# Optimization experiments

Measured on AMD Instinct MI355X. Metric: run time of the kernel, lower is better.

The kernel has to match this reference:

```python
import jax, jax.numpy as jnp
import numpy as np

B, H, L, N = 16, 128, 4096, 64
DT_MIN, DT_MAX = 0.001, 0.1


def _make_dplr_hippo(n):
    # NPLR HiPPO -> DPLR diagonalization (numpy, init-time only)
    p0 = np.sqrt(1 + 2 * np.arange(n))
    A = p0[:, None] * p0[None, :]
    A = -(np.tril(A) - np.diag(np.arange(n)))
    p = np.sqrt(np.arange(n) + 0.5)
    b = np.sqrt(2 * np.arange(n) + 1.0)
    S = A + p[:, None] * p[None, :]
    Lam_re = np.mean(np.diagonal(S)) * np.ones(n)
    Lam_im, V = np.linalg.eigh(S * -1j)
    p = V.conj().T @ p
    b = V.conj().T @ b
    return Lam_re + 1j * Lam_im, p, b


def setup_inputs() -> dict:
    key = jax.random.key(0)
    k1, k2, k3 = jax.random.split(key, 3)
    Lam, p, b = _make_dplr_hippo(N)
    tile = lambda a: jnp.tile(jnp.asarray(a, jnp.float32)[None], (H, 1))
    Lambda_re = tile(Lam.real)
    Lambda_im = tile(Lam.imag)
    P_ri = jnp.tile(jnp.stack([jnp.asarray(p.real, jnp.float32), jnp.asarray(p.imag, jnp.float32)], -1)[None], (H, 1, 1))
    B_ri = jnp.tile(jnp.stack([jnp.asarray(b.real, jnp.float32), jnp.asarray(b.imag, jnp.float32)], -1)[None], (H, 1, 1))
    C = (0.5 ** 0.5) * jax.random.normal(k1, (H, N, 2), jnp.float32)
    log_step = jax.random.uniform(k2, (H,)) * (np.log(DT_MAX) - np.log(DT_MIN)) + np.log(DT_MIN)
    D = jnp.ones((H,), jnp.float32)
    u = jax.random.normal(k3, (B, H, L), jnp.float32)
    return {"u": u, "Lambda_re": Lambda_re, "Lambda_im": Lambda_im, "P_ri": P_ri,
            "B_ri": B_ri, "C": C, "log_step": log_step.astype(jnp.float32), "D": D}


def reference(u, Lambda_re, Lambda_im, P_ri, B_ri, C, log_step, D):
    Lseq = u.shape[-1]
    # setup(): Lambda = clip(Lambda_re, max=-1e-4) + i*Lambda_im ; C complex ; step = exp(log_step)
    Lam = jnp.minimum(Lambda_re, -1e-4) + 1j * Lambda_im            # [H,N]
    P = P_ri[..., 0] + 1j * P_ri[..., 1]                             # [H,N]
    Bm = B_ri[..., 0] + 1j * B_ri[..., 1]                            # [H,N]
    Cc = C[..., 0] + 1j * C[..., 1]                                  # [H,N]
    step = jnp.exp(log_step)                                         # [H]
    # kernel_DPLR at the roots of unity
    Omega = jnp.exp(-2j * jnp.pi * (jnp.arange(Lseq) / Lseq))        # [L]
    g = (2.0 / step)[:, None] * ((1.0 - Omega) / (1.0 + Omega))[None, :]  # [H,L]
    c = 2.0 / (1.0 + Omega)                                          # [L]
    den = 1.0 / (g[:, :, None] - Lam[:, None, :])                    # [H,L,N] resolvent
    # four Cauchy dot products, batched: v stacked on last axis
    Vmat = jnp.stack([Cc.conj() * Bm, Cc.conj() * P, P.conj() * Bm, P.conj() * P], axis=-1)  # [H,N,4]
    Ks = jnp.einsum('hln,hnk->hlk', den, Vmat)                       # [H,L,4]
    k00, k01, k10, k11 = Ks[..., 0], Ks[..., 1], Ks[..., 2], Ks[..., 3]
    atRoots = c[None, :] * (k00 - k01 * (1.0 / (1.0 + k11)) * k10)   # [H,L]
    K = jnp.fft.ifft(atRoots, Lseq, axis=-1).real                    # [H,L] SSM kernel
    # causal FFT convolution: pad both to 2L
    ud = jnp.fft.rfft(jnp.pad(u, ((0, 0), (0, 0), (0, Lseq))), axis=-1)   # [B,H,L+1]
    Kd = jnp.fft.rfft(jnp.pad(K, ((0, 0), (0, Lseq))), axis=-1)           # [H,L+1]
    y = jnp.fft.irfft(ud * Kd[None], axis=-1)[..., :Lseq]            # [B,H,L]
    return y + D[None, :, None] * u
```

## Files before the change

### kernel.cpp

```cpp
#include <hip/hip_runtime.h>
#include <hip/hip_bf16.h>


#define PI_F 3.14159265358979323846f

__device__ __forceinline__ float2 cmulf(float2 a, float2 b) {
  return make_float2(a.x * b.x - a.y * b.y, a.x * b.y + a.y * b.x);
}
__device__ __forceinline__ void cmul_set(float2& v, float wr, float wi) {
  v = make_float2(v.x * wr - v.y * wi, v.x * wi + v.y * wr);
}
__device__ __forceinline__ int ad(int k) { return k + (k >> 4); }
__device__ __forceinline__ int sw16(int j) { return j ^ ((j >> 4) & 15); }

template <int SIGN>
__device__ __forceinline__ void bfly4(float2& a, float2& b, float2& c,
                                      float2& d) {
  float t0x = a.x + c.x, t0y = a.y + c.y;
  float t1x = a.x - c.x, t1y = a.y - c.y;
  float t2x = b.x + d.x, t2y = b.y + d.y;
  float t3x = b.x - d.x, t3y = b.y - d.y;
  a = make_float2(t0x + t2x, t0y + t2y);
  c = make_float2(t0x - t2x, t0y - t2y);
  if (SIGN < 0) {
    b = make_float2(t1x + t3y, t1y - t3x);
    d = make_float2(t1x - t3y, t1y + t3x);
  } else {
    b = make_float2(t1x - t3y, t1y + t3x);
    d = make_float2(t1x + t3y, t1y - t3x);
  }
}

template <int SIGN>
__device__ __forceinline__ void fft16(float2 v[16]) {
  const float sg = (float)SIGN;
  const float C1 = 0.92387953251128674f;
  const float S1 = 0.38268343236508978f;
  const float R2 = 0.70710678118654752f;
  bfly4<SIGN>(v[0], v[4], v[8], v[12]);
  bfly4<SIGN>(v[1], v[5], v[9], v[13]);
  bfly4<SIGN>(v[2], v[6], v[10], v[14]);
  bfly4<SIGN>(v[3], v[7], v[11], v[15]);
  cmul_set(v[5], C1, sg * S1);
  cmul_set(v[6], R2, sg * R2);
  cmul_set(v[7], S1, sg * C1);
  cmul_set(v[9], R2, sg * R2);
  v[10] = make_float2(-sg * v[10].y, sg * v[10].x);
  cmul_set(v[11], -R2, sg * R2);
  cmul_set(v[13], S1, sg * C1);
  cmul_set(v[14], -R2, sg * R2);
  cmul_set(v[15], -C1, -sg * S1);
  float2 w[16];
#pragma unroll
  for (int g = 0; g < 4; ++g) {
    float2 x0 = v[4 * g], x1 = v[4 * g + 1], x2 = v[4 * g + 2],
           x3 = v[4 * g + 3];
    bfly4<SIGN>(x0, x1, x2, x3);
    w[g] = x0; w[g + 4] = x1; w[g + 8] = x2; w[g + 12] = x3;
  }
#pragma unroll
  for (int i = 0; i < 16; ++i) v[i] = w[i];
}

__device__ __forceinline__ void tw_apply(float2 v[16], float ang) {
  float sn, cn;
  __sincosf(ang, &sn, &cn);
  float2 w1 = make_float2(cn, sn), cw = w1;
#pragma unroll
  for (int g = 1; g < 16; ++g) {
    v[g] = cmulf(v[g], cw);
    if (g < 15) cw = cmulf(cw, w1);
  }
}

template <int SIGN>
__device__ void fft4096_regs(float2 v[16], float2* lds, int tid) {
  const int a = tid & 15, g2 = tid >> 4;
  fft16<SIGN>(v);
  tw_apply(v, (float)SIGN * (2.0f * PI_F / 4096.0f) * (float)tid);
  __syncthreads();
#pragma unroll
  for (int g = 0; g < 16; ++g) lds[tid * 17 + g] = v[g];
  __syncthreads();
#pragma unroll
  for (int b = 0; b < 16; ++b) v[b] = lds[a * 17 + b * 272 + g2];
  fft16<SIGN>(v);
  tw_apply(v, (float)SIGN * (2.0f * PI_F / 256.0f) * (float)a);
  __syncthreads();
#pragma unroll
  for (int b = 0; b < 16; ++b) lds[g2 * 17 + b * 273 + a] = v[b];
  __syncthreads();
#pragma unroll
  for (int a2 = 0; a2 < 16; ++a2) v[a2] = lds[g2 * 17 + a * 273 + a2];
  fft16<SIGN>(v);
}

template <int SIGN>
__device__ void fft4096_regs_c(float2 v[16], float2* lds, int tid) {
  const int a = tid & 15, g2 = tid >> 4;
  fft16<SIGN>(v);
  tw_apply(v, (float)SIGN * (2.0f * PI_F / 4096.0f) * (float)tid);
  __syncthreads();
#pragma unroll
  for (int g = 0; g < 16; ++g) lds[(tid << 4) | (g ^ a)] = v[g];
  __syncthreads();
#pragma unroll
  for (int b = 0; b < 16; ++b) v[b] = lds[((a + 16 * b) << 4) | (g2 ^ a)];
  fft16<SIGN>(v);
  tw_apply(v, (float)SIGN * (2.0f * PI_F / 256.0f) * (float)a);
  __syncthreads();
#pragma unroll
  for (int b = 0; b < 16; ++b) lds[(g2 << 8) | (b << 4) | (a ^ b)] = v[b];
  __syncthreads();
#pragma unroll
  for (int a2 = 0; a2 < 16; ++a2) v[a2] = lds[(g2 << 8) | (a << 4) | (a2 ^ a)];
  fft16<SIGN>(v);
}

template <int SIGN>
__device__ void fft4096_scr2nat_c(float2 v[16], float2* lds, int tid) {
  const int a = tid & 15, g2 = tid >> 4;
  fft16<SIGN>(v);
  __syncthreads();
#pragma unroll
  for (int r = 0; r < 16; ++r) lds[(g2 << 8) | (a << 4) | (r ^ a)] = v[r];
  __syncthreads();
#pragma unroll
  for (int b = 0; b < 16; ++b) v[b] = lds[(g2 << 8) | (b << 4) | (a ^ b)];
  tw_apply(v, (float)SIGN * (2.0f * PI_F / 256.0f) * (float)a);
  fft16<SIGN>(v);
  __syncthreads();
#pragma unroll
  for (int r = 0; r < 16; ++r) lds[((16 * r + a) << 4) | (g2 ^ a)] = v[r];
  __syncthreads();
#pragma unroll
  for (int g = 0; g < 16; ++g) v[g] = lds[(tid << 4) | (g ^ a)];
  tw_apply(v, (float)SIGN * (2.0f * PI_F / 4096.0f) * (float)tid);
  fft16<SIGN>(v);
}

__global__ __launch_bounds__(256) void k_cauchy(
    const float* __restrict__ Lre, const float* __restrict__ Lim,
    const float* __restrict__ Pri, const float* __restrict__ Bri,
    const float* __restrict__ Cri, const float* __restrict__ lstep,
    float2* __restrict__ atR) {
  __shared__ float4 pA[64];
  __shared__ float4 pB[64];
  __shared__ float2 pL[64];
  const int h = blockIdx.x >> 4;
  const int sub = blockIdx.x & 15;
  const int tid = threadIdx.x;
  if (tid < 64) {
    int base = h * 64 + tid;
    float lr = fminf(Lre[base], -1e-4f);
    float li = Lim[base];
    float pr = Pri[2 * base], pi = Pri[2 * base + 1];
    float br = Bri[2 * base], bi = Bri[2 * base + 1];
    float cr = Cri[2 * base], ci = Cri[2 * base + 1];
    pA[tid] = make_float4(cr * br + ci * bi, cr * bi - ci * br,
                          cr * pr + ci * pi, cr * pi - ci * pr);
    pB[tid] = make_float4(pr * br + pi * bi, pr * bi - pi * br,
                          pr * pr + pi * pi, 0.f);
    pL[tid] = make_float2(lr, li);
  }
  __syncthreads();
  const float istep = expf(-lstep[h]);
  const int m = sub * 256 + tid;
  float sn, cn;
  __sincosf(-(2.0f * PI_F / 4096.0f) * (float)m, &sn, &cn);
  const float trm = 0.5f * (1.0f + cn);
  const float tim = 0.5f * sn;
  const float qrm = (1.0f - cn) * istep;
  const float qim = -sn * istep;
  float S0 = 0.f, S1 = 0.f, S2 = 0.f, S3 = 0.f, S4 = 0.f, S5 = 0.f, S6 = 0.f,
        S7 = 0.f;
#pragma unroll 8
  for (int n = 0; n < 64; ++n) {
    float4 a = pA[n];
    float4 b = pB[n];
    float2 L = pL[n];
    float dr = qrm - (trm * L.x - tim * L.y);
    float di = qim - (trm * L.y + tim * L.x);
    float inv = __builtin_amdgcn_rcpf(dr * dr + di * di);
    float sr = dr * inv, si = -di * inv;
    S0 += a.x * sr - a.y * si;  S1 += a.x * si + a.y * sr;
    S2 += a.z * sr - a.w * si;  S3 += a.z * si + a.w * sr;
    S4 += b.x * sr - b.y * si;  S5 += b.x * si + b.y * sr;
    S6 += b.z * sr;             S7 += b.z * si;
  }
  float tS11r = trm * S6 - tim * S7;
  float tS11i = trm * S7 + tim * S6;
  float denr = 1.0f + tS11r, deni = tS11i;
  float dinv = 1.0f / (denr * denr + deni * deni);
  float P1r = S2 * S4 - S3 * S5;
  float P1i = S2 * S5 + S3 * S4;
  float P2r = trm * P1r - tim * P1i;
  float P2i = trm * P1i + tim * P1r;
  float Qr = (P2r * denr + P2i * deni) * dinv;
  float Qi = (P2i * denr - P2r * deni) * dinv;
  atR[h * 4096 + m] = make_float2(S0 - Qr, S1 - Qi);
}

__global__ __launch_bounds__(256, 4) void k_khat(
    const float2* __restrict__ atR, const float* __restrict__ Dp,
    float4* __restrict__ abt) {
  __shared__ float2 lds[4368];
  const int h = blockIdx.x;
  const int tid = threadIdx.x;
  float2 v[16];
#pragma unroll
  for (int c = 0; c < 16; ++c) v[c] = atR[h * 4096 + tid + 256 * c];
  fft4096_regs<1>(v, lds, tid);
  const int kb = (tid >> 4) + 16 * (tid & 15);
  float* ldsf = (float*)lds;
  const float s = 1.0f / 4096.0f;
  __syncthreads();
#pragma unroll
  for (int al = 0; al < 16; ++al) ldsf[ad(kb + 256 * al)] = v[al].x * s;
  __syncthreads();
#pragma unroll
  for (int c = 0; c < 8; ++c) {
    int n = tid + 256 * c;
    v[c] = make_float2(ldsf[ad(2 * n)], ldsf[ad(2 * n + 1)]);
  }
#pragma unroll
  for (int c = 8; c < 16; ++c) v[c] = make_float2(0.f, 0.f);
  fft4096_regs<-1>(v, lds, tid);
  __syncthreads();
#pragma unroll
  for (int al = 0; al < 16; ++al) lds[ad(kb + 256 * al)] = v[al];
  __syncthreads();
  const float Dh = Dp[h];
#pragma unroll
  for (int c = 0; c < 16; ++c) {
    int k = kb + 256 * c;
    float2 Zk = lds[ad(k)];
    float2 Zm = lds[ad((4096 - k) & 4095)];
    float Er = 0.5f * (Zk.x + Zm.x), Ei = 0.5f * (Zk.y - Zm.y);
    float Or = 0.5f * (Zk.y + Zm.y), Oi = 0.5f * (Zm.x - Zk.x);
    float s_, c_;
    __sincosf(-(PI_F / 4096.0f) * (float)k, &s_, &c_);
    float Gr = c_ * Or - s_ * Oi, Gi = c_ * Oi + s_ * Or;
    float ar = (Er + Dh + s_ * Gr) * s;
    float ai = (Ei + s_ * Gi) * s;
    float br = (-c_ * Gi) * s;
    float bi = (c_ * Gr) * s;
    abt[h * 4096 + tid + 256 * c] = make_float4(ar, ai, br, bi);
  }
}

__global__ __launch_bounds__(256, 2) void k_conv(const float* __restrict__ u,
                                                 const float4* __restrict__ abt,
                                                 float* __restrict__ y) {
  __shared__ float2 lds[4096];
  const int r = blockIdx.x;
  const int h = r & 127;
  const int tid = threadIdx.x;
  const float2* u2 = (const float2*)(u + (size_t)r * 4096);
  float2 v[16];
#pragma unroll
  for (int c = 0; c < 8; ++c) v[c] = u2[tid + 256 * c];
#pragma unroll
  for (int c = 8; c < 16; ++c) v[c] = make_float2(0.f, 0.f);
  fft4096_regs_c<-1>(v, lds, tid);
  const int kb = (tid >> 4) + 16 * (tid & 15);
  __syncthreads();
#pragma unroll
  for (int al = 0; al < 16; ++al) lds[sw16(kb + 256 * al)] = v[al];
  __syncthreads();
  const float4* __restrict__ abrow = abt + h * 4096;
#pragma unroll
  for (int al = 0; al < 16; ++al) {
    int k = kb + 256 * al;
    float4 ab = abrow[tid + 256 * al];
    float2 Zm = lds[sw16((4096 - k) & 4095)];
    float2 Zk = v[al];
    v[al] = make_float2(ab.x * Zk.x - ab.y * Zk.y + ab.z * Zm.x + ab.w * Zm.y,
                        ab.x * Zk.y + ab.y * Zk.x + ab.w * Zm.x - ab.z * Zm.y);
  }
  fft4096_scr2nat_c<1>(v, lds, tid);
  float2* y2 = (float2*)(y + (size_t)r * 4096);
#pragma unroll
  for (int c = 0; c < 8; ++c) y2[tid + 256 * c] = v[c];
}

extern "C" void kernel_launch(void* const* d_in, const int* in_sizes, int n_in,
                              void* d_out, int out_size, void* d_ws,
                              size_t ws_size, hipStream_t stream) {
  (void)in_sizes; (void)n_in; (void)out_size; (void)ws_size;
  const float* u = (const float*)d_in[0];
  const float* Lre = (const float*)d_in[1];
  const float* Lim = (const float*)d_in[2];
  const float* Pri = (const float*)d_in[3];
  const float* Bri = (const float*)d_in[4];
  const float* Cri = (const float*)d_in[5];
  const float* lst = (const float*)d_in[6];
  const float* Dp = (const float*)d_in[7];
  float* y = (float*)d_out;
  float2* atR = (float2*)d_ws;
  float4* abt = (float4*)((char*)d_ws + (size_t)4 * 1024 * 1024);

  k_cauchy<<<2048, 256, 0, stream>>>(Lre, Lim, Pri, Bri, Cri, lst, atR);
  k_khat<<<128, 256, 0, stream>>>(atR, Dp, abt);
  k_conv<<<2048, 256, 0, stream>>>(u, abt, y);
}
```

Baseline: 157.5 us.

## Process two batch rows per conv block to share twiddles and kernel spectrum loads

```diff
diff --git a/kernel.cpp b/kernel.cpp
--- a/kernel.cpp
+++ b/kernel.cpp
@@ -73,6 +73,19 @@
   }
 }
 
+__device__ __forceinline__ void tw_apply2(float2 va[16], float2 vb[16],
+                                          float ang) {
+  float sn, cn;
+  __sincosf(ang, &sn, &cn);
+  float2 w1 = make_float2(cn, sn), cw = w1;
+#pragma unroll
+  for (int g = 1; g < 16; ++g) {
+    va[g] = cmulf(va[g], cw);
+    vb[g] = cmulf(vb[g], cw);
+    if (g < 15) cw = cmulf(cw, w1);
+  }
+}
+
 template <int SIGN>
 __device__ void fft4096_regs(float2 v[16], float2* lds, int tid) {
   const int a = tid & 15, g2 = tid >> 4;
@@ -96,47 +109,87 @@
 }
 
 template <int SIGN>
-__device__ void fft4096_regs_c(float2 v[16], float2* lds, int tid) {
+__device__ void fft4096_x2(float2 va[16], float2 vb[16], float2* A, float2* B,
+                           int tid) {
   const int a = tid & 15, g2 = tid >> 4;
-  fft16<SIGN>(v);
-  tw_apply(v, (float)SIGN * (2.0f * PI_F / 4096.0f) * (float)tid);
-  __syncthreads();
-#pragma unroll
-  for (int g = 0; g < 16; ++g) lds[(tid << 4) | (g ^ a)] = v[g];
-  __syncthreads();
-#pragma unroll
-  for (int b = 0; b < 16; ++b) v[b] = lds[((a + 16 * b) << 4) | (g2 ^ a)];
-  fft16<SIGN>(v);
-  tw_apply(v, (float)SIGN * (2.0f * PI_F / 256.0f) * (float)a);
-  __syncthreads();
-#pragma unroll
-  for (int b = 0; b < 16; ++b) lds[(g2 << 8) | (b << 4) | (a ^ b)] = v[b];
-  __syncthreads();
-#pragma unroll
-  for (int a2 = 0; a2 < 16; ++a2) v[a2] = lds[(g2 << 8) | (a << 4) | (a2 ^ a)];
-  fft16<SIGN>(v);
-}
-
-template <int SIGN>
-__device__ void fft4096_scr2nat_c(float2 v[16], float2* lds, int tid) {
+  fft16<SIGN>(va);
+  fft16<SIGN>(vb);
+  tw_apply2(va, vb, (float)SIGN * (2.0f * PI_F / 4096.0f) * (float)tid);
+  __syncthreads();
+#pragma unroll
+  for (int g = 0; g < 16; ++g) {
+    int s = (tid << 4) | (g ^ a);
+    A[s] = va[g];
+    B[s] = vb[g];
+  }
+  __syncthreads();
+#pragma unroll
+  for (int b = 0; b < 16; ++b) {
+    int s = ((a + 16 * b) << 4) | (g2 ^ a);
+    va[b] = A[s];
+    vb[b] = B[s];
+  }
+  fft16<SIGN>(va);
+  fft16<SIGN>(vb);
+  tw_apply2(va, vb, (float)SIGN * (2.0f * PI_F / 256.0f) * (float)a);
+  __syncthreads();
+#pragma unroll
+  for (int b = 0; b < 16; ++b) {
+    int s = (g2 << 8) | (b << 4) | (a ^ b);
+    A[s] = va[b];
+    B[s] = vb[b];
+  }
+  __syncthreads();
+#pragma unroll
+  for (int a2 = 0; a2 < 16; ++a2) {
+    int s = (g2 << 8) | (a << 4) | (a2 ^ a);
+    va[a2] = A[s];
+    vb[a2] = B[s];
+  }
+  fft16<SIGN>(va);
+  fft16<SIGN>(vb);
+}
+
+template <int SIGN>
+__device__ void fft4096_x2_s2n(float2 va[16], float2 vb[16], float2* A,
+                               float2* B, int tid) {
   const int a = tid & 15, g2 = tid >> 4;
-  fft16<SIGN>(v);
-  __syncthreads();
-#pragma unroll
-  for (int r = 0; r < 16; ++r) lds[(g2 << 8) | (a << 4) | (r ^ a)] = v[r];
-  __syncthreads();
-#pragma unroll
-  for (int b = 0; b < 16; ++b) v[b] = lds[(g2 << 8) | (b << 4) | (a ^ b)];
-  tw_apply(v, (float)SIGN * (2.0f * PI_F / 256.0f) * (float)a);
-  fft16<SIGN>(v);
-  __syncthreads();
-#pragma unroll
-  for (int r = 0; r < 16; ++r) lds[((16 * r + a) << 4) | (g2 ^ a)] = v[r];
-  __syncthreads();
-#pragma unroll
-  for (int g = 0; g < 16; ++g) v[g] = lds[(tid << 4) | (g ^ a)];
-  tw_apply(v, (float)SIGN * (2.0f * PI_F / 4096.0f) * (float)tid);
-  fft16<SIGN>(v);
+  fft16<SIGN>(va);
+  fft16<SIGN>(vb);
+  __syncthreads();
+#pragma unroll
+  for (int r = 0; r < 16; ++r) {
+    int s = (g2 << 8) | (a << 4) | (r ^ a);
+    A[s] = va[r];
+    B[s] = vb[r];
+  }
+  __syncthreads();
+#pragma unroll
+  for (int b = 0; b < 16; ++b) {
+    int s = (g2 << 8) | (b << 4) | (a ^ b);
+    va[b] = A[s];
+    vb[b] = B[s];
+  }
+  tw_apply2(va, vb, (float)SIGN * (2.0f * PI_F / 256.0f) * (float)a);
+  fft16<SIGN>(va);
+  fft16<SIGN>(vb);
+  __syncthreads();
+#pragma unroll
+  for (int r = 0; r < 16; ++r) {
+    int s = ((16 * r + a) << 4) | (g2 ^ a);
+    A[s] = va[r];
+    B[s] = vb[r];
+  }
+  __syncthreads();
+#pragma unroll
+  for (int g = 0; g < 16; ++g) {
+    int s = (tid << 4) | (g ^ a);
+    va[g] = A[s];
+    vb[g] = B[s];
+  }
+  tw_apply2(va, vb, (float)SIGN * (2.0f * PI_F / 4096.0f) * (float)tid);
+  fft16<SIGN>(va);
+  fft16<SIGN>(vb);
 }
 
 __global__ __launch_bounds__(256) void k_cauchy(
@@ -249,39 +302,63 @@
   }
 }
 
-__global__ __launch_bounds__(256, 2) void k_conv(const float* __restrict__ u,
-                                                 const float4* __restrict__ abt,
-                                                 float* __restrict__ y) {
-  __shared__ float2 lds[4096];
-  const int r = blockIdx.x;
-  const int h = r & 127;
+__global__ __launch_bounds__(256, 1) void k_conv2(
+    const float* __restrict__ u, const float4* __restrict__ abt,
+    float* __restrict__ y) {
+  __shared__ float2 lds[8192];
+  float2* A = lds;
+  float2* B = lds + 4096;
+  const int i = blockIdx.x;
+  const int h = i & 127;
   const int tid = threadIdx.x;
-  const float2* u2 = (const float2*)(u + (size_t)r * 4096);
-  float2 v[16];
-#pragma unroll
-  for (int c = 0; c < 8; ++c) v[c] = u2[tid + 256 * c];
-#pragma unroll
-  for (int c = 8; c < 16; ++c) v[c] = make_float2(0.f, 0.f);
-  fft4096_regs_c<-1>(v, lds, tid);
+  const float2* uA = (const float2*)(u + (size_t)i * 4096);
+  const float2* uB = (const float2*)(u + (size_t)(i + 1024) * 4096);
+  float2 va[16], vb[16];
+#pragma unroll
+  for (int c = 0; c < 8; ++c) {
+    va[c] = uA[tid + 256 * c];
+    vb[c] = uB[tid + 256 * c];
+  }
+#pragma unroll
+  for (int c = 8; c < 16; ++c) {
+    va[c] = make_float2(0.f, 0.f);
+    vb[c] = make_float2(0.f, 0.f);
+  }
+  fft4096_x2<-1>(va, vb, A, B, tid);
   const int kb = (tid >> 4) + 16 * (tid & 15);
   __syncthreads();
 #pragma unroll
-  for (int al = 0; al < 16; ++al) lds[sw16(kb + 256 * al)] = v[al];
+  for (int al = 0; al < 16; ++al) {
+    int s = sw16(kb + 256 * al);
+    A[s] = va[al];
+    B[s] = vb[al];
+  }
   __syncthreads();
   const float4* __restrict__ abrow = abt + h * 4096;
 #pragma unroll
   for (int al = 0; al < 16; ++al) {
     int k = kb + 256 * al;
+    int sp = sw16((4096 - k) & 4095);
     float4 ab = abrow[tid + 256 * al];
-    float2 Zm = lds[sw16((4096 - k) & 4095)];
-    float2 Zk = v[al];
-    v[al] = make_float2(ab.x * Zk.x - ab.y * Zk.y + ab.z * Zm.x + ab.w * Zm.y,
-                        ab.x * Zk.y + ab.y * Zk.x + ab.w * Zm.x - ab.z * Zm.y);
-  }
-  fft4096_scr2nat_c<1>(v, lds, tid);
-  float2* y2 = (float2*)(y + (size_t)r * 4096);
-#pragma unroll
-  for (int c = 0; c < 8; ++c) y2[tid + 256 * c] = v[c];
+    float2 Zma = A[sp];
+    float2 Zmb = B[sp];
+    float2 Za = va[al];
+    float2 Zb = vb[al];
+    va[al] =
+        make_float2(ab.x * Za.x - ab.y * Za.y + ab.z * Zma.x + ab.w * Zma.y,
+                    ab.x * Za.y + ab.y * Za.x + ab.w * Zma.x - ab.z * Zma.y);
+    vb[al] =
+        make_float2(ab.x * Zb.x - ab.y * Zb.y + ab.z * Zmb.x + ab.w * Zmb.y,
+                    ab.x * Zb.y + ab.y * Zb.x + ab.w * Zmb.x - ab.z * Zmb.y);
+  }
+  fft4096_x2_s2n<1>(va, vb, A, B, tid);
+  float2* yA = (float2*)(y + (size_t)i * 4096);
+  float2* yB = (float2*)(y + (size_t)(i + 1024) * 4096);
+#pragma unroll
+  for (int c = 0; c < 8; ++c) {
+    yA[tid + 256 * c] = va[c];
+    yB[tid + 256 * c] = vb[c];
+  }
 }
 
 extern "C" void kernel_launch(void* const* d_in, const int* in_sizes, int n_in,
@@ -302,5 +379,5 @@
 
   k_cauchy<<<2048, 256, 0, stream>>>(Lre, Lim, Pri, Bri, Cri, lst, atR);
   k_khat<<<128, 256, 0, stream>>>(atR, Dp, abt);
-  k_conv<<<2048, 256, 0, stream>>>(u, abt, y);
-}
+  k_conv2<<<1024, 256, 0, stream>>>(u, abt, y);
+}
```

Result: no change. 156.5 us (-0.6%).
